# Performance work log

Measured on AMD Instinct MI355X. Metric: run time of the kernel, lower is better.

## Reference

```python
import jax, jax.numpy as jnp
import numpy as np

N = 4096
D_IN = 1024
D_OUT = 1024
NUM_HEADS = 16
HEAD_DIM = D_OUT // NUM_HEADS


def setup_inputs() -> dict:
    key = jax.random.key(0)
    ks = jax.random.split(key, 7)
    scale = 1.0 / np.sqrt(D_IN)
    return {
        "q": jax.random.normal(ks[0], (N, D_IN), dtype=jnp.float32),
        "k": jax.random.normal(ks[1], (N, D_IN), dtype=jnp.float32),
        "v": jax.random.normal(ks[2], (N, D_IN), dtype=jnp.float32),
        "W_q": jax.random.normal(ks[3], (D_IN, D_OUT), dtype=jnp.float32) * scale,
        "W_k": jax.random.normal(ks[4], (D_IN, D_OUT), dtype=jnp.float32) * scale,
        "W_v": jax.random.normal(ks[5], (D_IN, D_OUT), dtype=jnp.float32) * scale,
        "W_o": jax.random.normal(ks[6], (D_OUT, D_OUT), dtype=jnp.float32) * scale,
    }


def reference(q, k, v, W_q, W_k, W_v, W_o):
    n = q.shape[0]
    # QKV projections -> [h, n, d]
    Q = (q @ W_q).reshape(n, NUM_HEADS, HEAD_DIM).transpose(1, 0, 2)
    K = (k @ W_k).reshape(n, NUM_HEADS, HEAD_DIM).transpose(1, 0, 2)
    V = (v @ W_v).reshape(n, NUM_HEADS, HEAD_DIM).transpose(1, 0, 2)
    scores = jnp.einsum('hid,hjd->hij', Q, K) / jnp.sqrt(jnp.float32(HEAD_DIM))
    attn = jax.nn.softmax(scores, axis=-1)  # dropout p=0.0 (eval) -> no-op
    h = jnp.einsum('hij,hjd->hid', attn, V)
    h = h.transpose(1, 0, 2).reshape(n, D_OUT)
    return h @ W_o
```

## Files before the change

kernel.cpp:

```cpp
#include <hip/hip_runtime.h>
#include <math.h>

#define NTOK   4096
#define DMODEL 1024
#define NHEADS 16
#define HDIM   64
#define KDIM   1024

typedef __attribute__((ext_vector_type(8))) short          bf16x8;
typedef __attribute__((ext_vector_type(4))) float          f32x4;
typedef __attribute__((ext_vector_type(16))) float         f32x16;
typedef __attribute__((ext_vector_type(4))) unsigned int   u32x4;
typedef __attribute__((ext_vector_type(4))) unsigned short us4;

static __device__ __forceinline__ unsigned short f2bf(float f) {
    unsigned int u = __float_as_uint(f);
    u += 0x7fffu + ((u >> 16) & 1u);
    return (unsigned short)(u >> 16);
}

static __device__ __forceinline__ unsigned int pk2bf(float a, float b) {
#if __has_builtin(__builtin_amdgcn_cvt_pk_bf16_f32)
    return __builtin_bit_cast(unsigned int,
                              __builtin_amdgcn_cvt_pk_bf16_f32(a, b));
#else
    unsigned int ua = __float_as_uint(a) + 0x8000u;
    unsigned int ub = __float_as_uint(b) + 0x8000u;
    return __builtin_amdgcn_perm(ub, ua, 0x07060302u);
#endif
}

#if __has_builtin(__builtin_amdgcn_exp2f)
#define EXP2(x) __builtin_amdgcn_exp2f(x)
#else
#define EXP2(x) exp2f(x)
#endif

static __device__ __forceinline__ void async_copy16(void* lds, const void* g) {
    __builtin_amdgcn_global_load_lds(
        (const __attribute__((address_space(1))) unsigned int*)g,
        (__attribute__((address_space(3))) unsigned int*)lds, 16, 0, 0);
}

static __device__ __forceinline__ unsigned int comb2(unsigned int x,
                                                     unsigned int y,
                                                     float inv) {
    float x0 = __uint_as_float(x << 16);
    float x1 = __uint_as_float(x & 0xffff0000u);
    float y0 = __uint_as_float(y << 16);
    float y1 = __uint_as_float(y & 0xffff0000u);
    return pk2bf((x0 + y0) * inv, (x1 + y1) * inv);
}

static __device__ __forceinline__ int xcd_swz(int flat, int nwg) {
    int cpx = nwg >> 3;
    return (flat & 7) * cpx + (flat >> 3);
}

#define CS_LD 136

static __device__ __forceinline__ void epi_rowmajor(
        unsigned short* Cs, unsigned short* Out, const f32x4 (&acc)[4][4],
        float sc, int wr, int wc, int quad, int l15, int t, int bm, int bn) {
    __syncthreads();
    #pragma unroll
    for (int mt = 0; mt < 4; mt++)
        #pragma unroll
        for (int nt = 0; nt < 4; nt++) {
            int col = wc * 64 + nt * 16 + l15;
            int row = wr * 64 + mt * 16 + quad * 4;
            #pragma unroll
            for (int r = 0; r < 4; r++)
                Cs[(row + r) * CS_LD + col] = f2bf(acc[mt][nt][r] * sc);
        }
    __syncthreads();
    #pragma unroll
    for (int p = 0; p < 8; p++) {
        int idx = p * 2048 + t * 8;
        int rl = idx >> 7, cl = idx & 127;
        uint4 v = *(const uint4*)(Cs + rl * CS_LD + cl);
        int n = bn + cl;
        *(uint4*)(Out + (size_t)(n >> 6) * NTOK * HDIM
                      + (size_t)(bm + rl) * HDIM + (n & 63)) = v;
    }
}

static __device__ __forceinline__ void epi_transposed(
        unsigned short* Cs, unsigned short* Out, const f32x4 (&acc)[4][4],
        int wr, int wc, int quad, int l15, int t, int bm, int bn) {
    __syncthreads();
    #pragma unroll
    for (int mt = 0; mt < 4; mt++)
        #pragma unroll
        for (int nt = 0; nt < 4; nt++) {
            int col = wc * 64 + nt * 16 + l15;
            int row = wr * 64 + mt * 16 + quad * 4;
            us4 o = { f2bf(acc[mt][nt][0]), f2bf(acc[mt][nt][1]),
                      f2bf(acc[mt][nt][2]), f2bf(acc[mt][nt][3]) };
            *(us4*)(Cs + col * CS_LD + row) = o;
        }
    __syncthreads();
    #pragma unroll
    for (int p = 0; p < 8; p++) {
        int idx = p * 2048 + t * 8;
        int cl = idx >> 7, rl = idx & 127;
        uint4 v = *(const uint4*)(Cs + cl * CS_LD + rl);
        int n = bn + cl;
        *(uint4*)(Out + (size_t)(n >> 6) * HDIM * NTOK
                      + (size_t)(n & 63) * NTOK + (bm + rl)) = v;
    }
}

__global__ __launch_bounds__(256)
void cast_wt_kernel(const float* __restrict__ Wq, const float* __restrict__ Wk,
                    const float* __restrict__ Wv, const float* __restrict__ Wo,
                    unsigned short* __restrict__ Tq, unsigned short* __restrict__ Tk,
                    unsigned short* __restrict__ Tv, unsigned short* __restrict__ To) {
    __shared__ float Ws[64][65];
    const float* W;
    unsigned short* T;
    switch (blockIdx.z) {
        case 0:  W = Wq; T = Tq; break;
        case 1:  W = Wk; T = Tk; break;
        case 2:  W = Wv; T = Tv; break;
        default: W = Wo; T = To; break;
    }
    const int k0 = blockIdx.x * 64, n0 = blockIdx.y * 64;
    const int t = threadIdx.x;
    #pragma unroll
    for (int i = 0; i < 4; i++) {
        int c  = i * 256 + t;
        int kk = c >> 4;
        int n4 = (c & 15) << 2;
        *(float4*)(&Ws[kk][n4]) =
            *(const float4*)(W + (size_t)(k0 + kk) * DMODEL + n0 + n4);
    }
    __syncthreads();
    #pragma unroll
    for (int i = 0; i < 4; i++) {
        int c  = i * 256 + t;
        int nn = c >> 4;
        int k4 = (c & 15) << 2;
        us4 o = { f2bf(Ws[k4 + 0][nn]), f2bf(Ws[k4 + 1][nn]),
                  f2bf(Ws[k4 + 2][nn]), f2bf(Ws[k4 + 3][nn]) };
        *(us4*)(T + (size_t)(n0 + nn) * KDIM + k0 + k4) = o;
    }
}

__global__ __launch_bounds__(256)
void cast_in_kernel(const float* __restrict__ q, const float* __restrict__ k,
                    const float* __restrict__ v,
                    unsigned short* __restrict__ Qb,
                    unsigned short* __restrict__ Kb,
                    unsigned short* __restrict__ Vb) {
    const float* src;
    unsigned short* dst;
    switch (blockIdx.y) {
        case 0:  src = q; dst = Qb; break;
        case 1:  src = k; dst = Kb; break;
        default: src = v; dst = Vb; break;
    }
    size_t i = ((size_t)blockIdx.x * 256 + threadIdx.x) * 8;
    float4 f0 = *(const float4*)(src + i);
    float4 f1 = *(const float4*)(src + i + 4);
    uint2 o0 = { pk2bf(f0.x, f0.y), pk2bf(f0.z, f0.w) };
    uint2 o1 = { pk2bf(f1.x, f1.y), pk2bf(f1.z, f1.w) };
    *(uint2*)(dst + i)     = o0;
    *(uint2*)(dst + i + 4) = o1;
}

__global__ __launch_bounds__(256, 3)
void qkv_gemm_pre(const unsigned short* __restrict__ Qb,
                  const unsigned short* __restrict__ Kb,
                  const unsigned short* __restrict__ Vb,
                  const unsigned short* __restrict__ Btq,
                  const unsigned short* __restrict__ Btk,
                  const unsigned short* __restrict__ Btv,
                  unsigned short* __restrict__ Oq, unsigned short* __restrict__ Ok,
                  unsigned short* __restrict__ Ov) {
    __shared__ __align__(16) unsigned short Sm[17408];
    unsigned short* As = Sm;
    unsigned short* Bs = Sm + 8192;

    const int flat = blockIdx.x + 8 * (blockIdx.y + 32 * blockIdx.z);
    const int id   = xcd_swz(flat, 768);
    const int bx   = id & 7;
    const int by   = (id >> 3) & 31;
    const int bz   = id >> 8;

    const unsigned short* A;
    const unsigned short* Bt;
    unsigned short* Out;
    int mode;
    float sc;
    switch (bz) {
        case 0:  A = Qb; Bt = Btq; Out = Oq; mode = 1; sc = 0.18033688011112042f; break;
        case 1:  A = Kb; Bt = Btk; Out = Ok; mode = 1; sc = 1.0f; break;
        default: A = Vb; Bt = Btv; Out = Ov; mode = 2; sc = 1.0f; break;
    }

    const int t    = threadIdx.x;
    const int w    = t >> 6;
    const int lane = t & 63;
    const int quad = lane >> 4;
    const int l15  = lane & 15;
    const int wr   = w >> 1, wc = w & 1;
    const int bm   = by * 128, bn = bx * 128;

    f32x4 acc[4][4];
    #pragma unroll
    for (int i = 0; i < 4; i++)
        #pragma unroll
        for (int j = 0; j < 4; j++) acc[i][j] = (f32x4)(0.f);

    for (int k0 = 0; k0 < KDIM; k0 += 64) {
        __syncthreads();
        #pragma unroll
        for (int i = 0; i < 4; i++) {
            int cb = (i * 4 + w) * 64;
            int c  = cb + lane;
            int r  = c >> 3;
            int ko = (c & 7) * 8;
            async_copy16((void*)(Bs + cb * 8),
                         (const void*)(Bt + (size_t)(bn + r) * KDIM + k0 + ko));
            async_copy16((void*)(As + cb * 8),
                         (const void*)(A + (size_t)(bm + r) * KDIM + k0 + ko));
        }
        __syncthreads();
        #pragma unroll
        for (int kq = 0; kq < 2; kq++) {
            bf16x8 af[4], bf[4];
            #pragma unroll
            for (int mt = 0; mt < 4; mt++)
                af[mt] = *(bf16x8*)(As + (wr * 64 + mt * 16 + l15) * 64 + kq * 32 + quad * 8);
            #pragma unroll
            for (int nt = 0; nt < 4; nt++)
                bf[nt] = *(bf16x8*)(Bs + (wc * 64 + nt * 16 + l15) * 64 + kq * 32 + quad * 8);
            #pragma unroll
            for (int mt = 0; mt < 4; mt++)
                #pragma unroll
                for (int nt = 0; nt < 4; nt++)
                    acc[mt][nt] = __builtin_amdgcn_mfma_f32_16x16x32_bf16(
                        af[mt], bf[nt], acc[mt][nt], 0, 0, 0);
        }
    }

    if (mode == 1)
        epi_rowmajor(Sm, Out, acc, sc, wr, wc, quad, l15, t, bm, bn);
    else
        epi_transposed(Sm, Out, acc, wr, wc, quad, l15, t, bm, bn);
}

__global__ __launch_bounds__(256, 3)
void qkv_gemm(const float* __restrict__ Aq, const float* __restrict__ Ak,
              const float* __restrict__ Av,
              const unsigned short* __restrict__ Btq,
              const unsigned short* __restrict__ Btk,
              const unsigned short* __restrict__ Btv,
              unsigned short* __restrict__ Oq, unsigned short* __restrict__ Ok,
              unsigned short* __restrict__ Ov) {
    __shared__ __align__(16) unsigned short Sm[17408];
    unsigned short* As = Sm;
    unsigned short* Bs = Sm + 8192;

    const float* A;
    const unsigned short* Bt;
    unsigned short* Out;
    int mode;
    float sc;
    switch (blockIdx.z) {
        case 0:  A = Aq; Bt = Btq; Out = Oq; mode = 1; sc = 0.18033688011112042f; break;
        case 1:  A = Ak; Bt = Btk; Out = Ok; mode = 1; sc = 1.0f; break;
        default: A = Av; Bt = Btv; Out = Ov; mode = 2; sc = 1.0f; break;
    }

    const int t    = threadIdx.x;
    const int w    = t >> 6;
    const int lane = t & 63;
    const int quad = lane >> 4;
    const int l15  = lane & 15;
    const int wr   = w >> 1, wc = w & 1;
    const int bm   = blockIdx.y * 128, bn = blockIdx.x * 128;

    f32x4 acc[4][4];
    #pragma unroll
    for (int i = 0; i < 4; i++)
        #pragma unroll
        for (int j = 0; j < 4; j++) acc[i][j] = (f32x4)(0.f);

    for (int k0 = 0; k0 < KDIM; k0 += 64) {
        __syncthreads();
        #pragma unroll
        for (int i = 0; i < 4; i++) {
            int cb = (i * 4 + w) * 64;
            int c  = cb + lane;
            int r  = c >> 3;
            int ko = (c & 7) * 8;
            async_copy16((void*)(Bs + cb * 8),
                         (const void*)(Bt + (size_t)(bn + r) * KDIM + k0 + ko));
        }
        #pragma unroll
        for (int i = 0; i < 4; i++) {
            int c2 = i * 256 + t;
            int r  = c2 >> 3;
            int k8 = (c2 & 7) * 8;
            const float* src = A + (size_t)(bm + r) * KDIM + k0 + k8;
            float4 f0 = *(const float4*)(src);
            float4 f1 = *(const float4*)(src + 4);
            uint2 p0 = { pk2bf(f0.x, f0.y), pk2bf(f0.z, f0.w) };
            uint2 p1 = { pk2bf(f1.x, f1.y), pk2bf(f1.z, f1.w) };
            *(uint2*)(As + r * 64 + k8)     = p0;
            *(uint2*)(As + r * 64 + k8 + 4) = p1;
        }
        __syncthreads();
        #pragma unroll
        for (int kq = 0; kq < 2; kq++) {
            bf16x8 af[4], bf[4];
            #pragma unroll
            for (int mt = 0; mt < 4; mt++)
                af[mt] = *(bf16x8*)(As + (wr * 64 + mt * 16 + l15) * 64 + kq * 32 + quad * 8);
            #pragma unroll
            for (int nt = 0; nt < 4; nt++)
                bf[nt] = *(bf16x8*)(Bs + (wc * 64 + nt * 16 + l15) * 64 + kq * 32 + quad * 8);
            #pragma unroll
            for (int mt = 0; mt < 4; mt++)
                #pragma unroll
                for (int nt = 0; nt < 4; nt++)
                    acc[mt][nt] = __builtin_amdgcn_mfma_f32_16x16x32_bf16(
                        af[mt], bf[nt], acc[mt][nt], 0, 0, 0);
        }
    }

    if (mode == 1)
        epi_rowmajor(Sm, Out, acc, sc, wr, wc, quad, l15, t, bm, bn);
    else
        epi_transposed(Sm, Out, acc, wr, wc, quad, l15, t, bm, bn);
}

__global__ __launch_bounds__(256, 3)
void out_gemm(const unsigned short* __restrict__ A,
              const unsigned short* __restrict__ Bt,
              float* __restrict__ Out) {
    __shared__ unsigned short As[64 * 64];
    __shared__ unsigned short Bs[128 * 64];

    const int t    = threadIdx.x;
    const int w    = t >> 6;
    const int lane = t & 63;
    const int quad = lane >> 4;
    const int l15  = lane & 15;
    const int wr   = w >> 1, wc = w & 1;
    const int bm   = blockIdx.y * 64, bn = blockIdx.x * 128;

    f32x4 acc[2][4];
    #pragma unroll
    for (int i = 0; i < 2; i++)
        #pragma unroll
        for (int j = 0; j < 4; j++) acc[i][j] = (f32x4)(0.f);

    for (int k0 = 0; k0 < KDIM; k0 += 64) {
        __syncthreads();
        #pragma unroll
        for (int i = 0; i < 4; i++) {
            int cb = (i * 4 + w) * 64;
            int c  = cb + lane;
            int r  = c >> 3;
            int ko = (c & 7) * 8;
            async_copy16((void*)(Bs + cb * 8),
                         (const void*)(Bt + (size_t)(bn + r) * KDIM + k0 + ko));
        }
        #pragma unroll
        for (int i = 0; i < 2; i++) {
            int cb = (i * 4 + w) * 64;
            int c  = cb + lane;
            int r  = c >> 3;
            int ko = (c & 7) * 8;
            async_copy16((void*)(As + cb * 8),
                         (const void*)(A + (size_t)(bm + r) * KDIM + k0 + ko));
        }
        __syncthreads();
        #pragma unroll
        for (int kq = 0; kq < 2; kq++) {
            bf16x8 af[2], bf[4];
            #pragma unroll
            for (int mt = 0; mt < 2; mt++)
                af[mt] = *(bf16x8*)(As + (wr * 32 + mt * 16 + l15) * 64 + kq * 32 + quad * 8);
            #pragma unroll
            for (int nt = 0; nt < 4; nt++)
                bf[nt] = *(bf16x8*)(Bs + (wc * 64 + nt * 16 + l15) * 64 + kq * 32 + quad * 8);
            #pragma unroll
            for (int mt = 0; mt < 2; mt++)
                #pragma unroll
                for (int nt = 0; nt < 4; nt++)
                    acc[mt][nt] = __builtin_amdgcn_mfma_f32_16x16x32_bf16(
                        af[mt], bf[nt], acc[mt][nt], 0, 0, 0);
        }
    }

    #pragma unroll
    for (int mt = 0; mt < 2; mt++) {
        #pragma unroll
        for (int nt = 0; nt < 4; nt++) {
            int col  = bn + wc * 64 + nt * 16 + l15;
            int row0 = bm + wr * 32 + mt * 16 + quad * 4;
            #pragma unroll
            for (int r = 0; r < 4; r++)
                Out[(size_t)(row0 + r) * DMODEL + col] = acc[mt][nt][r];
        }
    }
}

__global__ __launch_bounds__(256, 3)
void out_gemm_comb(const unsigned short* __restrict__ POa,
                   const float* __restrict__ lbuf,
                   const unsigned short* __restrict__ Bt,
                   float* __restrict__ Out) {
    __shared__ unsigned short As[64 * 64];
    __shared__ unsigned short Bs[128 * 64];

    const unsigned short* POb = POa + (size_t)NTOK * DMODEL;

    const int flat = blockIdx.x + 8 * blockIdx.y;
    const int id   = xcd_swz(flat, 512);
    const int bx   = id & 7;
    const int by   = id >> 3;

    const int t    = threadIdx.x;
    const int w    = t >> 6;
    const int lane = t & 63;
    const int quad = lane >> 4;
    const int l15  = lane & 15;
    const int wr   = w >> 1, wc = w & 1;
    const int bm   = by * 64, bn = bx * 128;

    f32x4 acc[2][4];
    #pragma unroll
    for (int i = 0; i < 2; i++)
        #pragma unroll
        for (int j = 0; j < 4; j++) acc[i][j] = (f32x4)(0.f);

    for (int k0 = 0; k0 < KDIM; k0 += 64) {
        __syncthreads();
        #pragma unroll
        for (int i = 0; i < 4; i++) {
            int cb = (i * 4 + w) * 64;
            int c  = cb + lane;
            int r  = c >> 3;
            int ko = (c & 7) * 8;
            async_copy16((void*)(Bs + cb * 8),
                         (const void*)(Bt + (size_t)(bn + r) * KDIM + k0 + ko));
        }
        #pragma unroll
        for (int i = 0; i < 2; i++) {
            int c   = i * 256 + t;
            int r   = c >> 3;
            int k8  = (c & 7) * 8;
            size_t row = (size_t)(bm + r);
            int col = k0 + k8;
            int hh  = col >> 6;
            uint4 a = *(const uint4*)(POa + row * DMODEL + col);
            uint4 b = *(const uint4*)(POb + row * DMODEL + col);
            float la = lbuf[(size_t)hh * NTOK + row];
            float lb = lbuf[(size_t)NHEADS * NTOK + (size_t)hh * NTOK + row];
            float inv = 1.f / (la + lb);
            uint4 o = { comb2(a.x, b.x, inv), comb2(a.y, b.y, inv),
                        comb2(a.z, b.z, inv), comb2(a.w, b.w, inv) };
            *(uint4*)(As + r * 64 + k8) = o;
        }
        __syncthreads();
        #pragma unroll
        for (int kq = 0; kq < 2; kq++) {
            bf16x8 af[2], bf[4];
            #pragma unroll
            for (int mt = 0; mt < 2; mt++)
                af[mt] = *(bf16x8*)(As + (wr * 32 + mt * 16 + l15) * 64 + kq * 32 + quad * 8);
            #pragma unroll
            for (int nt = 0; nt < 4; nt++)
                bf[nt] = *(bf16x8*)(Bs + (wc * 64 + nt * 16 + l15) * 64 + kq * 32 + quad * 8);
            #pragma unroll
            for (int mt = 0; mt < 2; mt++)
                #pragma unroll
                for (int nt = 0; nt < 4; nt++)
                    acc[mt][nt] = __builtin_amdgcn_mfma_f32_16x16x32_bf16(
                        af[mt], bf[nt], acc[mt][nt], 0, 0, 0);
        }
    }

    #pragma unroll
    for (int mt = 0; mt < 2; mt++) {
        #pragma unroll
        for (int nt = 0; nt < 4; nt++) {
            int col  = bn + wc * 64 + nt * 16 + l15;
            int row0 = bm + wr * 32 + mt * 16 + quad * 4;
            #pragma unroll
            for (int r = 0; r < 4; r++)
                Out[(size_t)(row0 + r) * DMODEL + col] = acc[mt][nt][r];
        }
    }
}

__global__ __launch_bounds__(256, 4)
void attn_split(const unsigned short* __restrict__ Q,
                const unsigned short* __restrict__ K,
                const unsigned short* __restrict__ Vt,
                unsigned short* __restrict__ PO,
                float* __restrict__ lbuf) {
    __shared__ __align__(16) unsigned short Ks[2 * 4096];
    __shared__ __align__(16) unsigned short Vs[2 * 4096];

    const int flat = blockIdx.x + 32 * (blockIdx.y + 16 * blockIdx.z);
    const int id   = xcd_swz(flat, 1024);
    const int qt   = id & 31;
    const int h    = (id >> 5) & 15;
    const int half = id >> 9;

    const int t    = threadIdx.x;
    const int w    = t >> 6;
    const int lane = t & 63;
    const int r    = lane & 31;
    const int hi   = lane >> 5;
    const int xh   = (r & 7) ^ hi;

    const unsigned short* Qg =
        Q + ((size_t)h * NTOK + qt * 128 + w * 32 + r) * HDIM + hi * 8;
    bf16x8 qf[4];
    #pragma unroll
    for (int ds = 0; ds < 4; ds++)
        qf[ds] = *(const bf16x8*)(Qg + ds * 16);

    const unsigned short* Kg = K  + ((size_t)h * NTOK + half * 2048) * HDIM;
    const unsigned short* Vg = Vt + (size_t)h * HDIM * NTOK + half * 2048;

    const int rr = t >> 3;
    const int oo = ((t & 7) ^ (rr & 7)) * 8;
    const unsigned short* kbase = Kg + (size_t)rr * HDIM + oo;
    const unsigned short* vbase = Vg + (size_t)rr * NTOK + oo;
    unsigned short* ksd = Ks + w * 512;
    unsigned short* vsd = Vs + w * 512;

    auto stage = [&](int kt, int b) {
        const unsigned short* kp = kbase + (size_t)kt * 64 * HDIM;
        const unsigned short* vp = vbase + kt * 64;
        async_copy16((void*)(ksd + b * 4096),        (const void*)kp);
        async_copy16((void*)(ksd + b * 4096 + 2048), (const void*)(kp + 32 * HDIM));
        async_copy16((void*)(vsd + b * 4096),        (const void*)vp);
        async_copy16((void*)(vsd + b * 4096 + 2048), (const void*)(vp + (size_t)32 * NTOK));
    };

    f32x16 O0 = (f32x16)(0.f), O1 = (f32x16)(0.f);
    float l0 = 0.f, l1 = 0.f, l2 = 0.f, l3 = 0.f;

    stage(0, 0);

    for (int kt = 0; kt < 32; kt++) {
        const int cur = kt & 1;
        __syncthreads();
        if (kt + 1 < 32) stage(kt + 1, cur ^ 1);

        const unsigned short* Kb = Ks + cur * 4096 + r * 64;
        const unsigned short* Vb = Vs + cur * 4096 + r * 64;

        f32x16 S0 = (f32x16)(0.f), S1 = (f32x16)(0.f);
        #pragma unroll
        for (int ds = 0; ds < 4; ds++) {
            int c = ((2 * ds) ^ xh) * 8;
            bf16x8 k0 = *(const bf16x8*)(Kb + c);
            bf16x8 k1 = *(const bf16x8*)(Kb + 2048 + c);
            S0 = __builtin_amdgcn_mfma_f32_32x32x16_bf16(k0, qf[ds], S0, 0, 0, 0);
            S1 = __builtin_amdgcn_mfma_f32_32x32x16_bf16(k1, qf[ds], S1, 0, 0, 0);
        }

        #pragma unroll
        for (int kb = 0; kb < 2; kb++) {
            const f32x16 S = kb ? S1 : S0;
            float p[16];
            #pragma unroll
            for (int i = 0; i < 16; i++) p[i] = EXP2(S[i]);
            #pragma unroll
            for (int i = 0; i < 4; i++) {
                l0 += p[i * 4 + 0];
                l1 += p[i * 4 + 1];
                l2 += p[i * 4 + 2];
                l3 += p[i * 4 + 3];
            }
            #pragma unroll
            for (int g = 0; g < 2; g++) {
                unsigned int w0 = pk2bf(p[g * 8 + 0], p[g * 8 + 1]);
                unsigned int w2 = pk2bf(p[g * 8 + 4], p[g * 8 + 5]);
                unsigned int w1 = pk2bf(p[g * 8 + 2], p[g * 8 + 3]);
                unsigned int w3 = pk2bf(p[g * 8 + 6], p[g * 8 + 7]);
                asm volatile("v_permlane32_swap_b32 %0, %1" : "+v"(w0), "+v"(w2));
                asm volatile("v_permlane32_swap_b32 %0, %1" : "+v"(w1), "+v"(w3));
                u32x4 pw = { w0, w1, w2, w3 };
                bf16x8 pf = __builtin_bit_cast(bf16x8, pw);
                int kg = kb * 2 + g;
                int c  = ((2 * kg) ^ xh) * 8;
                bf16x8 v0 = *(const bf16x8*)(Vb + c);
                bf16x8 v1 = *(const bf16x8*)(Vb + 2048 + c);
                O0 = __builtin_amdgcn_mfma_f32_32x32x16_bf16(v0, pf, O0, 0, 0, 0);
                O1 = __builtin_amdgcn_mfma_f32_32x32x16_bf16(v1, pf, O1, 0, 0, 0);
            }
        }
    }

    float lt  = (l0 + l1) + (l2 + l3);
    float ltot = lt + __shfl_xor(lt, 32, 64);

    unsigned short* POh = PO + (size_t)half * NTOK * DMODEL;
    size_t row = (size_t)qt * 128 + w * 32 + r;
    unsigned short* dst = POh + row * DMODEL + h * HDIM;
    #pragma unroll
    for (int db = 0; db < 2; db++) {
        const f32x16 O = db ? O1 : O0;
        #pragma unroll
        for (int g = 0; g < 4; g++) {
            int d = db * 32 + g * 8 + hi * 4;
            uint2 o = { pk2bf(O[g * 4 + 0], O[g * 4 + 1]),
                        pk2bf(O[g * 4 + 2], O[g * 4 + 3]) };
            *(uint2*)(dst + d) = o;
        }
    }
    if (hi == 0)
        lbuf[((size_t)half * NHEADS + h) * NTOK + row] = ltot;
}

__global__ __launch_bounds__(256)
void attn_mfma(const unsigned short* __restrict__ Q,
               const unsigned short* __restrict__ K,
               const unsigned short* __restrict__ Vt,
               unsigned short* __restrict__ ctx) {
    __shared__ __align__(16) unsigned short Ks[2 * 4096];
    __shared__ __align__(16) unsigned short Vs[2 * 4096];
    __shared__ __align__(16) unsigned short Ps[4][32][72];

    const int h    = blockIdx.y;
    const int qt   = blockIdx.x;
    const int t    = threadIdx.x;
    const int w    = t >> 6;
    const int lane = t & 63;
    const int quad = lane >> 4;
    const int l15  = lane & 15;

    const unsigned short* Qg =
        Q + ((size_t)h * NTOK + qt * 128 + w * 32 + l15) * HDIM;
    bf16x8 qf[2][2];
    qf[0][0] = *(const bf16x8*)(Qg + quad * 8);
    qf[0][1] = *(const bf16x8*)(Qg + 32 + quad * 8);
    qf[1][0] = *(const bf16x8*)(Qg + 16 * HDIM + quad * 8);
    qf[1][1] = *(const bf16x8*)(Qg + 16 * HDIM + 32 + quad * 8);

    const unsigned short* Kg = K  + (size_t)h * NTOK * HDIM;
    const unsigned short* Vg = Vt + (size_t)h * HDIM * NTOK;

    const int rr = t >> 3;
    const int oo = ((t & 7) ^ (rr & 7)) * 8;
    const unsigned short* kbase = Kg + (size_t)rr * HDIM + oo;
    const unsigned short* vbase = Vg + (size_t)rr * NTOK + oo;
    unsigned short* ksd = Ks + w * 512;
    unsigned short* vsd = Vs + w * 512;

    auto stage = [&](int kt, int b) {
        const unsigned short* kp = kbase + (size_t)kt * 64 * HDIM;
        const unsigned short* vp = vbase + kt * 64;
        async_copy16((void*)(ksd + b * 4096),        (const void*)kp);
        async_copy16((void*)(ksd + b * 4096 + 2048), (const void*)(kp + 32 * HDIM));
        async_copy16((void*)(vsd + b * 4096),        (const void*)vp);
        async_copy16((void*)(vsd + b * 4096 + 2048), (const void*)(vp + (size_t)32 * NTOK));
    };

    const int xb = l15 & 7;
    const int a0 = l15 * 64 + ((quad    ) ^ xb) * 8;
    const int a1 = l15 * 64 + ((quad + 4) ^ xb) * 8;

    const bf16x8 ones = { 16256, 16256, 16256, 16256,
                          16256, 16256, 16256, 16256 };

    f32x4 O[2][4];
    f32x4 lacc[2];
    #pragma unroll
    for (int tl = 0; tl < 2; tl++) {
        lacc[tl] = (f32x4)(0.f);
        #pragma unroll
        for (int dt = 0; dt < 4; dt++) O[tl][dt] = (f32x4)(0.f);
    }

    stage(0, 0);

    for (int kt = 0; kt < NTOK / 64; kt++) {
        const int cur = kt & 1;
        __syncthreads();
        if (kt + 1 < NTOK / 64) stage(kt + 1, cur ^ 1);

        f32x4 s[2][4];
        #pragma unroll
        for (int kc = 0; kc < 4; kc++) {
            bf16x8 kf0 = *(bf16x8*)(Ks + cur * 4096 + kc * 1024 + a0);
            bf16x8 kf1 = *(bf16x8*)(Ks + cur * 4096 + kc * 1024 + a1);
            #pragma unroll
            for (int tl = 0; tl < 2; tl++) {
                f32x4 acc = (f32x4)(0.f);
                acc = __builtin_amdgcn_mfma_f32_16x16x32_bf16(kf0, qf[tl][0], acc, 0, 0, 0);
                acc = __builtin_amdgcn_mfma_f32_16x16x32_bf16(kf1, qf[tl][1], acc, 0, 0, 0);
                s[tl][kc] = acc;
            }
        }

        bf16x8 vf[4][2];
        #pragma unroll
        for (int dt = 0; dt < 4; dt++) {
            vf[dt][0] = *(bf16x8*)(Vs + cur * 4096 + dt * 1024 + a0);
            vf[dt][1] = *(bf16x8*)(Vs + cur * 4096 + dt * 1024 + a1);
        }

        #pragma unroll
        for (int tl = 0; tl < 2; tl++) {
            #pragma unroll
            for (int kc = 0; kc < 4; kc++) {
                float e0 = EXP2(s[tl][kc][0]);
                float e1 = EXP2(s[tl][kc][1]);
                float e2 = EXP2(s[tl][kc][2]);
                float e3 = EXP2(s[tl][kc][3]);
                uint2 p = { pk2bf(e0, e1), pk2bf(e2, e3) };
                *(uint2*)(&Ps[w][tl * 16 + l15][kc * 16 + quad * 4]) = p;
            }
            asm volatile("s_waitcnt lgkmcnt(0)" ::: "memory");

            bf16x8 pf0 = *(bf16x8*)(&Ps[w][tl * 16 + l15][quad * 8]);
            bf16x8 pf1 = *(bf16x8*)(&Ps[w][tl * 16 + l15][32 + quad * 8]);
            lacc[tl] = __builtin_amdgcn_mfma_f32_16x16x32_bf16(ones, pf0, lacc[tl], 0, 0, 0);
            lacc[tl] = __builtin_amdgcn_mfma_f32_16x16x32_bf16(ones, pf1, lacc[tl], 0, 0, 0);
            #pragma unroll
            for (int dt = 0; dt < 4; dt++) {
                O[tl][dt] = __builtin_amdgcn_mfma_f32_16x16x32_bf16(vf[dt][0], pf0, O[tl][dt], 0, 0, 0);
                O[tl][dt] = __builtin_amdgcn_mfma_f32_16x16x32_bf16(vf[dt][1], pf1, O[tl][dt], 0, 0, 0);
            }
        }
    }

    #pragma unroll
    for (int tl = 0; tl < 2; tl++) {
        float inv = 1.f / lacc[tl][0];
        size_t row = (size_t)qt * 128 + w * 32 + tl * 16 + l15;
        #pragma unroll
        for (int dt = 0; dt < 4; dt++) {
            uint2 o = { pk2bf(O[tl][dt][0] * inv, O[tl][dt][1] * inv),
                        pk2bf(O[tl][dt][2] * inv, O[tl][dt][3] * inv) };
            *(uint2*)(ctx + row * DMODEL + h * HDIM + dt * 16 + quad * 4) = o;
        }
    }
}

extern "C" void kernel_launch(void* const* d_in, const int* in_sizes, int n_in,
                              void* d_out, int out_size, void* d_ws, size_t ws_size,
                              hipStream_t stream) {
    const float* q  = (const float*)d_in[0];
    const float* k  = (const float*)d_in[1];
    const float* v  = (const float*)d_in[2];
    const float* Wq = (const float*)d_in[3];
    const float* Wk = (const float*)d_in[4];
    const float* Wv = (const float*)d_in[5];
    const float* Wo = (const float*)d_in[6];
    float* out = (float*)d_out;

    unsigned short* WqT = (unsigned short*)d_ws;
    unsigned short* WkT = WqT + (size_t)DMODEL * KDIM;
    unsigned short* WvT = WkT + (size_t)DMODEL * KDIM;
    unsigned short* WoT = WvT + (size_t)DMODEL * KDIM;
    unsigned short* Qh  = WoT + (size_t)DMODEL * KDIM;
    unsigned short* Kh  = Qh  + (size_t)NTOK * DMODEL;
    unsigned short* Vth = Kh  + (size_t)NTOK * DMODEL;
    unsigned short* ctx = Vth + (size_t)NTOK * DMODEL;
    unsigned short* Qb  = ctx + (size_t)NTOK * DMODEL;
    unsigned short* Kb  = Qb  + (size_t)NTOK * DMODEL;
    unsigned short* Vb  = Kb  + (size_t)NTOK * DMODEL;
    unsigned short* PO  = Qb;
    float*          lb  = (float*)(PO + (size_t)2 * NTOK * DMODEL);

    const bool bigws = ws_size >= (size_t)67108864;

    cast_wt_kernel<<<dim3(16, 16, 4), 256, 0, stream>>>(Wq, Wk, Wv, Wo,
                                                        WqT, WkT, WvT, WoT);
    if (bigws) {
        cast_in_kernel<<<dim3(2048, 3), 256, 0, stream>>>(q, k, v, Qb, Kb, Vb);
        qkv_gemm_pre<<<dim3(DMODEL / 128, NTOK / 128, 3), 256, 0, stream>>>(
            Qb, Kb, Vb, WqT, WkT, WvT, Qh, Kh, Vth);
        attn_split<<<dim3(NTOK / 128, NHEADS, 2), 256, 0, stream>>>(
            Qh, Kh, Vth, PO, lb);
        out_gemm_comb<<<dim3(DMODEL / 128, NTOK / 64), 256, 0, stream>>>(
            PO, lb, WoT, out);
    } else {
        qkv_gemm<<<dim3(DMODEL / 128, NTOK / 128, 3), 256, 0, stream>>>(
            q, k, v, WqT, WkT, WvT, Qh, Kh, Vth);
        attn_mfma<<<dim3(NTOK / 128, NHEADS), 256, 0, stream>>>(Qh, Kh, Vth, ctx);
        out_gemm<<<dim3(DMODEL / 128, NTOK / 64), 256, 0, stream>>>(ctx, WoT, out);
    }
}
```

Baseline: 253.3 us.

## Double-buffer pre-converted QKV GEMM loads and raise MFMA priority in attention

The bf16 QKV GEMM (qkv_gemm_pre) now uses a two-stage shared-memory double buffer with K-step 32 and one barrier per iteration, so the next tile's async copies overlap the current MFMAs. In the attention kernel, the first QK MFMA takes a zero constant instead of zeroing the accumulator first, and the MFMA sections are wrapped in s_setprio to favour matrix issue across waves. The aims are to hide global-load latency in the GEMM and to keep the matrix units busy in attention. The trade-off is half-size K-steps, which double the loop iterations and barriers.

```diff
diff --git a/kernel.cpp b/kernel.cpp
--- a/kernel.cpp
+++ b/kernel.cpp
@@ -179,8 +179,8 @@
                   unsigned short* __restrict__ Oq, unsigned short* __restrict__ Ok,
                   unsigned short* __restrict__ Ov) {
     __shared__ __align__(16) unsigned short Sm[17408];
-    unsigned short* As = Sm;
-    unsigned short* Bs = Sm + 8192;
+    unsigned short* AsP = Sm;
+    unsigned short* BsP = Sm + 8192;
 
     const int flat = blockIdx.x + 8 * (blockIdx.y + 32 * blockIdx.z);
     const int id   = xcd_swz(flat, 768);
@@ -207,42 +207,48 @@
     const int wr   = w >> 1, wc = w & 1;
     const int bm   = by * 128, bn = bx * 128;
 
+    const int sr  = w * 16 + (lane >> 2);
+    const int sko = (lane & 3) * 8;
+    const unsigned short* Abase = A  + (size_t)(bm + sr) * KDIM + sko;
+    const unsigned short* Bbase = Bt + (size_t)(bn + sr) * KDIM + sko;
+
+    auto stage = [&](int k0, int b) {
+        unsigned short* ad = AsP + b * 4096 + w * 512;
+        unsigned short* bd = BsP + b * 4096 + w * 512;
+        async_copy16((void*)(ad),        (const void*)(Abase + k0));
+        async_copy16((void*)(ad + 2048), (const void*)(Abase + (size_t)64 * KDIM + k0));
+        async_copy16((void*)(bd),        (const void*)(Bbase + k0));
+        async_copy16((void*)(bd + 2048), (const void*)(Bbase + (size_t)64 * KDIM + k0));
+    };
+
     f32x4 acc[4][4];
     #pragma unroll
     for (int i = 0; i < 4; i++)
         #pragma unroll
         for (int j = 0; j < 4; j++) acc[i][j] = (f32x4)(0.f);
 
-    for (int k0 = 0; k0 < KDIM; k0 += 64) {
+    stage(0, 0);
+
+    for (int it = 0; it < 32; it++) {
+        const int cur = it & 1;
         __syncthreads();
-        #pragma unroll
-        for (int i = 0; i < 4; i++) {
-            int cb = (i * 4 + w) * 64;
-            int c  = cb + lane;
-            int r  = c >> 3;
-            int ko = (c & 7) * 8;
-            async_copy16((void*)(Bs + cb * 8),
-                         (const void*)(Bt + (size_t)(bn + r) * KDIM + k0 + ko));
-            async_copy16((void*)(As + cb * 8),
-                         (const void*)(A + (size_t)(bm + r) * KDIM + k0 + ko));
-        }
-        __syncthreads();
-        #pragma unroll
-        for (int kq = 0; kq < 2; kq++) {
-            bf16x8 af[4], bf[4];
-            #pragma unroll
-            for (int mt = 0; mt < 4; mt++)
-                af[mt] = *(bf16x8*)(As + (wr * 64 + mt * 16 + l15) * 64 + kq * 32 + quad * 8);
+        if (it + 1 < 32) stage((it + 1) * 32, cur ^ 1);
+
+        const unsigned short* Ab = AsP + cur * 4096;
+        const unsigned short* Bb = BsP + cur * 4096;
+        bf16x8 af[4], bf[4];
+        #pragma unroll
+        for (int mt = 0; mt < 4; mt++)
+            af[mt] = *(const bf16x8*)(Ab + (wr * 64 + mt * 16 + l15) * 32 + quad * 8);
+        #pragma unroll
+        for (int nt = 0; nt < 4; nt++)
+            bf[nt] = *(const bf16x8*)(Bb + (wc * 64 + nt * 16 + l15) * 32 + quad * 8);
+        #pragma unroll
+        for (int mt = 0; mt < 4; mt++)
             #pragma unroll
             for (int nt = 0; nt < 4; nt++)
-                bf[nt] = *(bf16x8*)(Bs + (wc * 64 + nt * 16 + l15) * 64 + kq * 32 + quad * 8);
-            #pragma unroll
-            for (int mt = 0; mt < 4; mt++)
-                #pragma unroll
-                for (int nt = 0; nt < 4; nt++)
-                    acc[mt][nt] = __builtin_amdgcn_mfma_f32_16x16x32_bf16(
-                        af[mt], bf[nt], acc[mt][nt], 0, 0, 0);
-        }
+                acc[mt][nt] = __builtin_amdgcn_mfma_f32_16x16x32_bf16(
+                    af[mt], bf[nt], acc[mt][nt], 0, 0, 0);
     }
 
     if (mode == 1)
@@ -547,6 +553,7 @@
         async_copy16((void*)(vsd + b * 4096 + 2048), (const void*)(vp + (size_t)32 * NTOK));
     };
 
+    const f32x16 Zf = (f32x16)(0.f);
     f32x16 O0 = (f32x16)(0.f), O1 = (f32x16)(0.f);
     float l0 = 0.f, l1 = 0.f, l2 = 0.f, l3 = 0.f;
 
@@ -560,15 +567,24 @@
         const unsigned short* Kb = Ks + cur * 4096 + r * 64;
         const unsigned short* Vb = Vs + cur * 4096 + r * 64;
 
-        f32x16 S0 = (f32x16)(0.f), S1 = (f32x16)(0.f);
-        #pragma unroll
-        for (int ds = 0; ds < 4; ds++) {
+        f32x16 S0, S1;
+        __builtin_amdgcn_s_setprio(1);
+        {
+            int c = ((0) ^ xh) * 8;
+            bf16x8 k0 = *(const bf16x8*)(Kb + c);
+            bf16x8 k1 = *(const bf16x8*)(Kb + 2048 + c);
+            S0 = __builtin_amdgcn_mfma_f32_32x32x16_bf16(k0, qf[0], Zf, 0, 0, 0);
+            S1 = __builtin_amdgcn_mfma_f32_32x32x16_bf16(k1, qf[0], Zf, 0, 0, 0);
+        }
+        #pragma unroll
+        for (int ds = 1; ds < 4; ds++) {
             int c = ((2 * ds) ^ xh) * 8;
             bf16x8 k0 = *(const bf16x8*)(Kb + c);
             bf16x8 k1 = *(const bf16x8*)(Kb + 2048 + c);
             S0 = __builtin_amdgcn_mfma_f32_32x32x16_bf16(k0, qf[ds], S0, 0, 0, 0);
             S1 = __builtin_amdgcn_mfma_f32_32x32x16_bf16(k1, qf[ds], S1, 0, 0, 0);
         }
+        __builtin_amdgcn_s_setprio(0);
 
         #pragma unroll
         for (int kb = 0; kb < 2; kb++) {
@@ -597,8 +613,10 @@
                 int c  = ((2 * kg) ^ xh) * 8;
                 bf16x8 v0 = *(const bf16x8*)(Vb + c);
                 bf16x8 v1 = *(const bf16x8*)(Vb + 2048 + c);
+                __builtin_amdgcn_s_setprio(1);
                 O0 = __builtin_amdgcn_mfma_f32_32x32x16_bf16(v0, pf, O0, 0, 0, 0);
                 O1 = __builtin_amdgcn_mfma_f32_32x32x16_bf16(v1, pf, O1, 0, 0, 0);
+                __builtin_amdgcn_s_setprio(0);
             }
         }
     }
```

Result: no change. 256.2 us (+1.1%).
